# Performance work log

Measured on AMD Instinct MI355X. Metric: run time of the kernel, lower is better.

## Reference

```python
import jax, jax.numpy as jnp
import numpy as np

HIDDEN = 5120
NH = 32
DQ = 128    # qk nope dim
DR = 64     # qk rope dim
DV = 128    # v head dim
Q_LORA = 1536
KV_LORA = 512
T = 2048
THETA = 10000.0
EPS = 1e-6


def rmsnorm(x, g, eps=EPS):
    return x * jax.lax.rsqrt(jnp.mean(x * x, axis=-1, keepdims=True) + eps) * g


def rotate_gptj(x):
    # interleaved pairs: (x0, x1) -> (-x1, x0)
    x1 = x[..., ::2]
    x2 = x[..., 1::2]
    return jnp.stack((-x2, x1), axis=-1).reshape(x.shape)


def setup_inputs() -> dict:
    key = jax.random.key(0)
    ks = jax.random.split(key, 8)
    s = 0.02
    return {
        'positions': jnp.arange(T, dtype=jnp.int32),
        'hidden_states': jax.random.normal(ks[0], (T, HIDDEN), jnp.float32),
        'w_qa': jax.random.normal(ks[1], (HIDDEN, Q_LORA), jnp.float32) * s,
        'gamma_q': jnp.ones((Q_LORA,), jnp.float32),
        'w_qb': jax.random.normal(ks[2], (Q_LORA, NH * (DQ + DR)), jnp.float32) * s,
        'w_kva': jax.random.normal(ks[3], (HIDDEN, KV_LORA + DR), jnp.float32) * s,
        'gamma_kv': jnp.ones((KV_LORA,), jnp.float32),
        'w_kvb': jax.random.normal(ks[4], (KV_LORA, NH * (DQ + DV)), jnp.float32) * s,
        'w_o': jax.random.normal(ks[5], (NH * DV, HIDDEN), jnp.float32) * s,
    }


def reference(positions, hidden_states, w_qa, gamma_q, w_qb, w_kva, gamma_kv, w_kvb, w_o):
    t = hidden_states.shape[0]
    # --- Q path: low-rank down-proj, RMSNorm, up-proj ---
    q_c = rmsnorm(hidden_states @ w_qa, gamma_q)               # [T, Q_LORA]
    q = (q_c @ w_qb).reshape(t, NH, DQ + DR)                   # [T, H, 192]
    q_nope, q_pe = q[..., :DQ], q[..., DQ:]
    # --- KV path: joint down-proj, split latent / rope key, RMSNorm latent ---
    kv = hidden_states @ w_kva                                 # [T, KV_LORA + DR]
    kv_c, k_pe = kv[:, :KV_LORA], kv[:, KV_LORA:]
    kv_c = rmsnorm(kv_c, gamma_kv)
    kv_up = (kv_c @ w_kvb).reshape(t, NH, DQ + DV)             # [T, H, 256]
    k_nope, v = kv_up[..., :DQ], kv_up[..., DQ:]
    # --- partial RoPE (GPT-J rotate, neox-style cos/sin cache) ---
    inv_freq = 1.0 / (THETA ** (jnp.arange(0, DR, 2, dtype=jnp.float32) / DR))
    freqs = positions.astype(jnp.float32)[:, None] * inv_freq  # [T, DR/2]
    emb = jnp.concatenate((freqs, freqs), axis=-1)             # [T, DR]
    cos = jnp.cos(emb)[:, None, :]                             # [T, 1, DR]
    sin = jnp.sin(emb)[:, None, :]
    q_pe = q_pe * cos + rotate_gptj(q_pe) * sin                # [T, H, DR]
    k_pe = k_pe[:, None, :]
    k_pe = k_pe * cos + rotate_gptj(k_pe) * sin                # [T, 1, DR]
    # --- attention ---
    q_full = jnp.concatenate((q_nope, q_pe), axis=-1)                          # [T, H, 192]
    k_full = jnp.concatenate((k_nope, jnp.broadcast_to(k_pe, (t, NH, DR))), axis=-1)
    scale = (DQ + DR) ** -0.5
    scores = jnp.einsum('qhd,khd->hqk', q_full, k_full) * scale                # [H, T, T]
    causal = positions[:, None] >= positions[None, :]
    scores = jnp.where(causal[None], scores, jnp.float32(-1e30))
    attn = jax.nn.softmax(scores, axis=-1)
    out = jnp.einsum('hqk,khd->qhd', attn, v).reshape(t, NH * DV)              # [T, H*DV]
    return out @ w_o                                                           # [T, HIDDEN]
```

## Files before the change

### kernel.cpp

```cpp
#include <hip/hip_runtime.h>
#include <hip/hip_bf16.h>
#include <cstdint>
#include <cstddef>

#define T_SEQ   2048
#define HIDDEN  5120
#define NH      32
#define DQ      128
#define DR      64
#define DV      128
#define Q_LORA  1536
#define KV_LORA 512
#define QD      (DQ + DR)
#define KVD     (KV_LORA + DR)
#define QROW    (NH * QD)
#define KVUPROW (NH * (DQ + DV))
#define AOROW   (NH * DV)
#define FUSED_N (Q_LORA + KVD)
#define FUSED_PE (Q_LORA + KV_LORA)

typedef short bf16x8 __attribute__((ext_vector_type(8)));
typedef float f32x4  __attribute__((ext_vector_type(4)));

#define GLOAD16(gp, lp)                                                        \
    __builtin_amdgcn_global_load_lds(                                          \
        (const __attribute__((address_space(1))) void*)(gp),                   \
        (__attribute__((address_space(3))) void*)(lp), 16, 0, 0)

static __device__ __forceinline__ short f2bf(float f)
{
    union { float f; unsigned u; } v; v.f = f;
    unsigned r = v.u + 0x7FFFu + ((v.u >> 16) & 1u);
    return (short)(r >> 16);
}
static __device__ __forceinline__ float bf2f(short s)
{
    union { unsigned u; float f; } v;
    v.u = ((unsigned)(unsigned short)s) << 16;
    return v.f;
}

__global__ __launch_bounds__(256) void zero_f32(float* __restrict__ p, int n4)
{
    const int stride = gridDim.x * 256;
    for (int i = blockIdx.x * 256 + threadIdx.x; i < n4; i += stride)
        ((float4*)p)[i] = make_float4(0.f, 0.f, 0.f, 0.f);
}

__global__ __launch_bounds__(256) void conv_bf(
    const float* __restrict__ src, short* __restrict__ dst)
{
    const size_t i = ((size_t)blockIdx.x * 256 + threadIdx.x) * 8;
    float4 a = *(const float4*)&src[i];
    float4 b = *(const float4*)&src[i + 4];
    union { short s[8]; uint4 u; } o;
    o.s[0] = f2bf(a.x); o.s[1] = f2bf(a.y); o.s[2] = f2bf(a.z); o.s[3] = f2bf(a.w);
    o.s[4] = f2bf(b.x); o.s[5] = f2bf(b.y); o.s[6] = f2bf(b.z); o.s[7] = f2bf(b.w);
    *(uint4*)&dst[i] = o.u;
}

__global__ __launch_bounds__(256) void tr_f32_bf16(
    const float* __restrict__ src, short* __restrict__ dst, int K, int N)
{
    const int k0 = blockIdx.x * 32, n0 = blockIdx.y * 32;
    __shared__ float t[32][33];
    const int tid = threadIdx.x;
    {
        const int r = tid >> 3, c4 = (tid & 7) * 4;
        float4 v = *(const float4*)&src[(size_t)(k0 + r) * N + n0 + c4];
        t[r][c4 + 0] = v.x; t[r][c4 + 1] = v.y;
        t[r][c4 + 2] = v.z; t[r][c4 + 3] = v.w;
    }
    __syncthreads();
    {
        const int n = tid >> 3, k4 = (tid & 7) * 4;
        union { short s[4]; uint2 u; } o;
#pragma unroll
        for (int j = 0; j < 4; ++j) o.s[j] = f2bf(t[k4 + j][n]);
        *(uint2*)&dst[(size_t)(n0 + n) * K + k0 + k4] = o.u;
    }
}

__global__ __launch_bounds__(256, 4) void gemm_bt(
    const short* __restrict__ A, const short* __restrict__ BT,
    float* __restrict__ Cf, short* __restrict__ Cb, int N, int K,
    int lda, int ldbt, int ldc)
{
    __shared__ short As[128 * 64];
    __shared__ short Bs[128 * 64];

    const int gx = gridDim.x;
    const int nwg = gx * gridDim.y;
    int flat = blockIdx.y * gx + blockIdx.x;
    if ((nwg & 7) == 0) {
        const int chunk = nwg >> 3;
        flat = (flat & 7) * chunk + (flat >> 3);
    }
    const int bm = (flat / gx) * 128;
    const int bn = (flat % gx) * 128;

    const int kchunk = K / gridDim.z;
    const int kbeg   = kchunk * blockIdx.z;
    const int kend   = kbeg + kchunk;

    const int tid  = threadIdx.x;
    const int w    = tid >> 6;
    const int l    = tid & 63;
    const int wm   = (w >> 1) * 64;
    const int wn   = (w & 1) * 64;
    const int quad = l >> 4;
    const int lrow = l & 15;

    f32x4 acc[4][4];
#pragma unroll
    for (int mt = 0; mt < 4; ++mt)
#pragma unroll
        for (int nt = 0; nt < 4; ++nt)
            acc[mt][nt] = (f32x4){0.f, 0.f, 0.f, 0.f};

    const int r0  = tid >> 3;
    const int c8  = (tid & 7) * 8;
    const int rbA = bm + r0;
    int rbB = bn + r0; if (rbB > N - 1) rbB = N - 1;

    for (int k0 = kbeg; k0 < kend; k0 += 64) {
        __syncthreads();
#pragma unroll
        for (int i = 0; i < 4; ++i) {
            const int r = r0 + 32 * i;
            GLOAD16(&A[(size_t)(rbA + 32 * i) * lda + k0 + c8], &As[r * 64 + c8]);
        }
#pragma unroll
        for (int i = 0; i < 4; ++i) {
            const int r  = r0 + 32 * i;
            int rb = rbB + 32 * i; if (rb > N - 1) rb = N - 1;
            GLOAD16(&BT[(size_t)rb * ldbt + k0 + c8], &Bs[r * 64 + c8]);
        }
        __syncthreads();

#pragma unroll
        for (int ks = 0; ks < 2; ++ks) {
            bf16x8 af[4], bfr[4];
#pragma unroll
            for (int mt = 0; mt < 4; ++mt)
                af[mt] = *(const bf16x8*)&As[(wm + mt * 16 + lrow) * 64 + ks * 32 + quad * 8];
#pragma unroll
            for (int nt = 0; nt < 4; ++nt)
                bfr[nt] = *(const bf16x8*)&Bs[(wn + nt * 16 + lrow) * 64 + ks * 32 + quad * 8];
#pragma unroll
            for (int mt = 0; mt < 4; ++mt)
#pragma unroll
                for (int nt = 0; nt < 4; ++nt)
                    acc[mt][nt] = __builtin_amdgcn_mfma_f32_16x16x32_bf16(
                        af[mt], bfr[nt], acc[mt][nt], 0, 0, 0);
        }
    }

    if (Cb == nullptr) {
        const bool atom = (gridDim.z > 1);
#pragma unroll
        for (int mt = 0; mt < 4; ++mt)
#pragma unroll
            for (int i = 0; i < 4; ++i) {
                const int row = bm + wm + mt * 16 + quad * 4 + i;
                float* crow = Cf + (size_t)row * ldc;
#pragma unroll
                for (int nt = 0; nt < 4; ++nt) {
                    const int col = bn + wn + nt * 16 + lrow;
                    if (col < N) {
                        if (atom) atomicAdd(&crow[col], acc[mt][nt][i]);
                        else      crow[col] = acc[mt][nt][i];
                    }
                }
            }
    } else {
#pragma unroll
        for (int mt = 0; mt < 4; ++mt)
#pragma unroll
            for (int i = 0; i < 4; ++i) {
                const int row = bm + wm + mt * 16 + quad * 4 + i;
                short* crow = Cb + (size_t)row * ldc;
#pragma unroll
                for (int nt = 0; nt < 4; ++nt) {
                    const int col = bn + wn + nt * 16 + lrow;
                    if (col < N) crow[col] = f2bf(acc[mt][nt][i]);
                }
            }
    }
}

__global__ __launch_bounds__(256, 4) void gemm_kv(
    const short* __restrict__ A, const short* __restrict__ BT,
    short* __restrict__ Kg, short* __restrict__ Vg)
{
    __shared__ short As[128 * 64];
    __shared__ short Bs[128 * 64];

    const int gx = gridDim.x;
    const int nwg = gx * gridDim.y;
    int flat = blockIdx.y * gx + blockIdx.x;
    if ((nwg & 7) == 0) {
        const int chunk = nwg >> 3;
        flat = (flat & 7) * chunk + (flat >> 3);
    }
    const int bm = (flat / gx) * 128;
    const int bn = (flat % gx) * 128;

    const int tid  = threadIdx.x;
    const int w    = tid >> 6;
    const int l    = tid & 63;
    const int wm   = (w >> 1) * 64;
    const int wn   = (w & 1) * 64;
    const int quad = l >> 4;
    const int lrow = l & 15;

    f32x4 acc[4][4];
#pragma unroll
    for (int mt = 0; mt < 4; ++mt)
#pragma unroll
        for (int nt = 0; nt < 4; ++nt)
            acc[mt][nt] = (f32x4){0.f, 0.f, 0.f, 0.f};

    const int r0 = tid >> 3;
    const int c8 = (tid & 7) * 8;

    for (int k0 = 0; k0 < KV_LORA; k0 += 64) {
        __syncthreads();
#pragma unroll
        for (int i = 0; i < 4; ++i) {
            const int r = r0 + 32 * i;
            GLOAD16(&A[(size_t)(bm + r) * KV_LORA + k0 + c8], &As[r * 64 + c8]);
        }
#pragma unroll
        for (int i = 0; i < 4; ++i) {
            const int r = r0 + 32 * i;
            GLOAD16(&BT[(size_t)(bn + r) * KV_LORA + k0 + c8], &Bs[r * 64 + c8]);
        }
        __syncthreads();

#pragma unroll
        for (int ks = 0; ks < 2; ++ks) {
            bf16x8 af[4], bfr[4];
#pragma unroll
            for (int mt = 0; mt < 4; ++mt)
                af[mt] = *(const bf16x8*)&As[(wm + mt * 16 + lrow) * 64 + ks * 32 + quad * 8];
#pragma unroll
            for (int nt = 0; nt < 4; ++nt)
                bfr[nt] = *(const bf16x8*)&Bs[(wn + nt * 16 + lrow) * 64 + ks * 32 + quad * 8];
#pragma unroll
            for (int mt = 0; mt < 4; ++mt)
#pragma unroll
                for (int nt = 0; nt < 4; ++nt)
                    acc[mt][nt] = __builtin_amdgcn_mfma_f32_16x16x32_bf16(
                        af[mt], bfr[nt], acc[mt][nt], 0, 0, 0);
        }
    }

    const int  h     = bn >> 8;
    const bool vhalf = (bn & 128) != 0;
    if (!vhalf) {
        short* KgH = Kg + (size_t)h * (2048 * 192);
#pragma unroll
        for (int mt = 0; mt < 4; ++mt)
#pragma unroll
            for (int i = 0; i < 4; ++i) {
                const int row = bm + wm + mt * 16 + quad * 4 + i;
#pragma unroll
                for (int nt = 0; nt < 4; ++nt) {
                    const int d = wn + nt * 16 + lrow;
                    KgH[(size_t)row * 192 + d] = f2bf(acc[mt][nt][i]);
                }
            }
    } else {
        short* VgH = Vg + (size_t)h * (128 * 2048);
#pragma unroll
        for (int mt = 0; mt < 4; ++mt)
#pragma unroll
            for (int nt = 0; nt < 4; ++nt) {
                const int dv   = wn + nt * 16 + lrow;
                const int rowb = bm + wm + mt * 16 + quad * 4;
                union { short s[4]; uint2 u; } t;
                t.s[0] = f2bf(acc[mt][nt][0]); t.s[1] = f2bf(acc[mt][nt][1]);
                t.s[2] = f2bf(acc[mt][nt][2]); t.s[3] = f2bf(acc[mt][nt][3]);
                *(uint2*)&VgH[(size_t)dv * 2048 + rowb] = t.u;
            }
    }
}

__global__ __launch_bounds__(256) void rmsnorm_bf(
    const float* __restrict__ x, const float* __restrict__ g,
    short* __restrict__ y, int len, int in_stride, int out_stride)
{
    const float* xr = x + (size_t)blockIdx.x * in_stride;
    short*       yr = y + (size_t)blockIdx.x * out_stride;
    float ss = 0.f;
    for (int i = threadIdx.x; i < len; i += 256) {
        float v = xr[i];
        ss += v * v;
    }
#pragma unroll
    for (int off = 32; off > 0; off >>= 1) ss += __shfl_down(ss, off);
    __shared__ float red[4];
    if ((threadIdx.x & 63) == 0) red[threadIdx.x >> 6] = ss;
    __syncthreads();
    float tot = red[0] + red[1] + red[2] + red[3];
    float scale = rsqrtf(tot / (float)len + 1e-6f);
    for (int i = threadIdx.x; i < len; i += 256)
        yr[i] = f2bf(xr[i] * scale * g[i]);
}

#define ROPE_LN_THETA_OVER_32 0.28782313662425575f

__device__ __forceinline__ void rope_pair(float p, int i, float& x0, float& x1)
{
    const int   j0 = (2 * i) & 31;
    const int   j1 = (2 * i + 1) & 31;
    const float a0 = p * expf(-(float)j0 * ROPE_LN_THETA_OVER_32);
    const float a1 = p * expf(-(float)j1 * ROPE_LN_THETA_OVER_32);
    const float r0 = x0 * cosf(a0) - x1 * sinf(a0);
    const float r1 = x1 * cosf(a1) + x0 * sinf(a1);
    x0 = r0; x1 = r1;
}

__global__ __launch_bounds__(256) void rope_q_bf(
    short* __restrict__ qb, const int* __restrict__ pos)
{
    const int idx = blockIdx.x * 256 + threadIdx.x;
    const int i = idx & 31;
    const int h = (idx >> 5) & 31;
    const int t = idx >> 10;
    short* base = qb + (size_t)t * QROW + h * QD + DQ;
    float x0 = bf2f(base[2 * i]), x1 = bf2f(base[2 * i + 1]);
    rope_pair((float)pos[t], i, x0, x1);
    union { short s[2]; unsigned u; } o;
    o.s[0] = f2bf(x0); o.s[1] = f2bf(x1);
    *(unsigned*)&base[2 * i] = o.u;
}

__global__ __launch_bounds__(256) void rope_k_bcast(
    const float* __restrict__ qkva, const int* __restrict__ pos,
    short* __restrict__ Kg)
{
    const int idx = blockIdx.x * 256 + threadIdx.x;
    const int i = idx & 31;
    const int t = idx >> 5;
    const float* base = qkva + (size_t)t * FUSED_N + FUSED_PE;
    float x0 = base[2 * i], x1 = base[2 * i + 1];
    rope_pair((float)pos[t], i, x0, x1);
    union { short s[2]; unsigned u; } pk;
    pk.s[0] = f2bf(x0); pk.s[1] = f2bf(x1);
    for (int h = 0; h < NH; ++h)
        *(unsigned*)&Kg[((size_t)h * 2048 + t) * 192 + 128 + 2 * i] = pk.u;
}

__global__ __launch_bounds__(256) void attn_mfma(
    const short* __restrict__ qb, const short* __restrict__ Kg,
    const short* __restrict__ Vg, short* __restrict__ aout)
{
    const int h  = blockIdx.x;
    const int qb_ = blockIdx.y;
    const int q0 = qb_ * 64;

    __shared__ short Qs[64 * 200];
    __shared__ short Ks[64 * 200];
    __shared__ short Vt[128 * 72];
    __shared__ short Ps[64 * 72];

    const int tid  = threadIdx.x;
    const int w    = tid >> 6;
    const int l    = tid & 63;
    const int quad = l >> 4;
    const int lrow = l & 15;

    const float scale = 0.07216878364870322f;

#pragma unroll
    for (int it = 0; it < 6; ++it) {
        const int id = tid + 256 * it;
        const int r = id / 24, g = id % 24;
        *(uint4*)&Qs[r * 200 + g * 8] =
            *(const uint4*)&qb[(size_t)(q0 + r) * QROW + h * QD + g * 8];
    }
    __syncthreads();

    bf16x8 afq[6];
#pragma unroll
    for (int ks = 0; ks < 6; ++ks)
        afq[ks] = *(const bf16x8*)&Qs[(w * 16 + lrow) * 200 + ks * 32 + quad * 8];

    f32x4 Oacc[8];
#pragma unroll
    for (int nt = 0; nt < 8; ++nt) Oacc[nt] = (f32x4){0.f, 0.f, 0.f, 0.f};
    float m_run[4] = {-1e30f, -1e30f, -1e30f, -1e30f};
    float l_run[4] = {0.f, 0.f, 0.f, 0.f};

    const short* KgH = Kg + (size_t)h * (2048 * 192);
    const short* VgH = Vg + (size_t)h * (128 * 2048);

    for (int kt = 0; kt <= qb_; ++kt) {
        __syncthreads();
#pragma unroll
        for (int it = 0; it < 6; ++it) {
            const int id = tid + 256 * it;
            const int r = id / 24, g = id % 24;
            *(uint4*)&Ks[r * 200 + g * 8] =
                *(const uint4*)&KgH[(size_t)(kt * 64 + r) * 192 + g * 8];
        }
#pragma unroll
        for (int it = 0; it < 4; ++it) {
            const int id = tid + 256 * it;
            const int rv = id >> 3, g = id & 7;
            *(uint4*)&Vt[rv * 72 + g * 8] =
                *(const uint4*)&VgH[(size_t)rv * 2048 + kt * 64 + g * 8];
        }
        __syncthreads();

        f32x4 Sc[4];
#pragma unroll
        for (int nt = 0; nt < 4; ++nt) Sc[nt] = (f32x4){0.f, 0.f, 0.f, 0.f};
#pragma unroll
        for (int ks = 0; ks < 6; ++ks)
#pragma unroll
            for (int nt = 0; nt < 4; ++nt) {
                bf16x8 bk = *(const bf16x8*)&Ks[(nt * 16 + lrow) * 200 + ks * 32 + quad * 8];
                Sc[nt] = __builtin_amdgcn_mfma_f32_16x16x32_bf16(afq[ks], bk, Sc[nt], 0, 0, 0);
            }
#pragma unroll
        for (int nt = 0; nt < 4; ++nt)
#pragma unroll
            for (int i = 0; i < 4; ++i) Sc[nt][i] *= scale;

        if (kt == qb_) {
            const int qrow = w * 16 + quad * 4;
#pragma unroll
            for (int nt = 0; nt < 4; ++nt)
#pragma unroll
                for (int i = 0; i < 4; ++i)
                    if (nt * 16 + lrow > qrow + i) Sc[nt][i] = -1e30f;
        }

        float alpha[4];
#pragma unroll
        for (int i = 0; i < 4; ++i) {
            float m = fmaxf(fmaxf(Sc[0][i], Sc[1][i]), fmaxf(Sc[2][i], Sc[3][i]));
            m = fmaxf(m, __shfl_xor(m, 1));
            m = fmaxf(m, __shfl_xor(m, 2));
            m = fmaxf(m, __shfl_xor(m, 4));
            m = fmaxf(m, __shfl_xor(m, 8));
            const float mn = fmaxf(m_run[i], m);
            alpha[i] = expf(m_run[i] - mn);
            m_run[i] = mn;
        }

        float rs[4] = {0.f, 0.f, 0.f, 0.f};
#pragma unroll
        for (int nt = 0; nt < 4; ++nt)
#pragma unroll
            for (int i = 0; i < 4; ++i) {
                const float p = expf(Sc[nt][i] - m_run[i]);
                rs[i] += p;
                Ps[(w * 16 + quad * 4 + i) * 72 + nt * 16 + lrow] = f2bf(p);
            }
#pragma unroll
        for (int i = 0; i < 4; ++i) {
            float r = rs[i];
            r += __shfl_xor(r, 1);
            r += __shfl_xor(r, 2);
            r += __shfl_xor(r, 4);
            r += __shfl_xor(r, 8);
            l_run[i] = l_run[i] * alpha[i] + r;
        }

#pragma unroll
        for (int nt = 0; nt < 8; ++nt)
#pragma unroll
            for (int i = 0; i < 4; ++i) Oacc[nt][i] *= alpha[i];

#pragma unroll
        for (int ks2 = 0; ks2 < 2; ++ks2) {
            bf16x8 ap = *(const bf16x8*)&Ps[(w * 16 + lrow) * 72 + ks2 * 32 + quad * 8];
#pragma unroll
            for (int nt = 0; nt < 8; ++nt) {
                bf16x8 bv = *(const bf16x8*)&Vt[(nt * 16 + lrow) * 72 + ks2 * 32 + quad * 8];
                Oacc[nt] = __builtin_amdgcn_mfma_f32_16x16x32_bf16(ap, bv, Oacc[nt], 0, 0, 0);
            }
        }
    }

    float invl[4];
#pragma unroll
    for (int i = 0; i < 4; ++i) invl[i] = 1.f / l_run[i];
#pragma unroll
    for (int nt = 0; nt < 8; ++nt)
#pragma unroll
        for (int i = 0; i < 4; ++i)
            aout[(size_t)(q0 + w * 16 + quad * 4 + i) * AOROW + h * 128 + nt * 16 + lrow]
                = f2bf(Oacc[nt][i] * invl[i]);
}

extern "C" void kernel_launch(void* const* d_in, const int* in_sizes, int n_in,
                              void* d_out, int out_size, void* d_ws, size_t ws_size,
                              hipStream_t stream)
{
    const int*   positions = (const int*)d_in[0];
    const float* hidden    = (const float*)d_in[1];
    const float* w_qa      = (const float*)d_in[2];
    const float* gamma_q   = (const float*)d_in[3];
    const float* w_qb      = (const float*)d_in[4];
    const float* w_kva     = (const float*)d_in[5];
    const float* gamma_kv  = (const float*)d_in[6];
    const float* w_kvb     = (const float*)d_in[7];
    const float* w_o       = (const float*)d_in[8];
    float*       out       = (float*)d_out;

    short* wT      = (short*)d_ws;
    short* hid_bf  = wT      + (size_t)20971520;
    short* qbuf_bf = hid_bf  + (size_t)T_SEQ * HIDDEN;
    short* Kg      = qbuf_bf + (size_t)T_SEQ * QROW;
    short* Vg      = Kg      + (size_t)NH * 2048 * 192;
    short* aout_bf = Vg      + (size_t)NH * 128 * 2048;
    short* qa_bf   = aout_bf + (size_t)T_SEQ * AOROW;
    short* kvc_bf  = qa_bf   + (size_t)T_SEQ * Q_LORA;
    float* qkva    = (float*)Vg;

    const dim3 blk(256);

    zero_f32<<<dim3(2048), blk, 0, stream>>>(qkva, T_SEQ * FUSED_N / 4);
    zero_f32<<<dim3(2048), blk, 0, stream>>>(out, T_SEQ * HIDDEN / 4);
    conv_bf<<<dim3(T_SEQ * HIDDEN / 8 / 256), blk, 0, stream>>>(hidden, hid_bf);

    tr_f32_bf16<<<dim3(HIDDEN / 32, Q_LORA / 32), blk, 0, stream>>>(w_qa, wT, HIDDEN, Q_LORA);
    tr_f32_bf16<<<dim3(HIDDEN / 32, KVD / 32), blk, 0, stream>>>(
        w_kva, wT + (size_t)Q_LORA * HIDDEN, HIDDEN, KVD);
    gemm_bt<<<dim3((FUSED_N + 127) / 128, T_SEQ / 128, 2), blk, 0, stream>>>(
        hid_bf, wT, qkva, nullptr, FUSED_N, HIDDEN, HIDDEN, HIDDEN, FUSED_N);

    rmsnorm_bf<<<dim3(T_SEQ), blk, 0, stream>>>(qkva, gamma_q, qa_bf, Q_LORA, FUSED_N, Q_LORA);
    rmsnorm_bf<<<dim3(T_SEQ), blk, 0, stream>>>(qkva + Q_LORA, gamma_kv, kvc_bf,
                                                KV_LORA, FUSED_N, KV_LORA);
    rope_k_bcast<<<dim3(T_SEQ * 32 / 256), blk, 0, stream>>>(qkva, positions, Kg);

    tr_f32_bf16<<<dim3(Q_LORA / 32, QROW / 32), blk, 0, stream>>>(w_qb, wT, Q_LORA, QROW);
    gemm_bt<<<dim3(QROW / 128, T_SEQ / 128, 1), blk, 0, stream>>>(
        qa_bf, wT, nullptr, qbuf_bf, QROW, Q_LORA, Q_LORA, Q_LORA, QROW);

    tr_f32_bf16<<<dim3(KV_LORA / 32, KVUPROW / 32), blk, 0, stream>>>(w_kvb, wT, KV_LORA, KVUPROW);
    gemm_kv<<<dim3(KVUPROW / 128, T_SEQ / 128), blk, 0, stream>>>(kvc_bf, wT, Kg, Vg);

    rope_q_bf<<<dim3(T_SEQ * NH * 32 / 256), blk, 0, stream>>>(qbuf_bf, positions);

    attn_mfma<<<dim3(NH, T_SEQ / 64), blk, 0, stream>>>(qbuf_bf, Kg, Vg, aout_bf);

    tr_f32_bf16<<<dim3(AOROW / 32, HIDDEN / 32), blk, 0, stream>>>(w_o, wT, AOROW, HIDDEN);
    gemm_bt<<<dim3(HIDDEN / 128, T_SEQ / 128, 2), blk, 0, stream>>>(
        aout_bf, wT, out, nullptr, HIDDEN, AOROW, AOROW, AOROW, HIDDEN);
}
```

Measured before the change: 758.7 us.

## Prefetch next K/V tile into registers, fold scale into exp2, reverse block order

```diff
diff --git a/kernel.cpp b/kernel.cpp
--- a/kernel.cpp
+++ b/kernel.cpp
@@ -357,11 +357,10 @@
     const short* __restrict__ qb, const short* __restrict__ Kg,
     const short* __restrict__ Vg, short* __restrict__ aout)
 {
-    const int h  = blockIdx.x;
-    const int qb_ = blockIdx.y;
-    const int q0 = qb_ * 64;
-
-    __shared__ short Qs[64 * 200];
+    const int h   = blockIdx.x;
+    const int qb_ = gridDim.y - 1 - blockIdx.y;
+    const int q0  = qb_ * 64;
+
     __shared__ short Ks[64 * 200];
     __shared__ short Vt[128 * 72];
     __shared__ short Ps[64 * 72];
@@ -372,30 +371,38 @@
     const int quad = l >> 4;
     const int lrow = l & 15;
 
-    const float scale = 0.07216878364870322f;
-
+    const float K2 = 0.104117547f;
+
+    bf16x8 afq[6];
+    {
+        const short* qrow = qb + (size_t)(q0 + w * 16 + lrow) * QROW + h * QD;
+#pragma unroll
+        for (int ks = 0; ks < 6; ++ks)
+            afq[ks] = *(const bf16x8*)&qrow[ks * 32 + quad * 8];
+    }
+
+    f32x4 Oacc[8];
+#pragma unroll
+    for (int nt = 0; nt < 8; ++nt) Oacc[nt] = (f32x4){0.f, 0.f, 0.f, 0.f};
+    float m_run[4] = {-1e30f, -1e30f, -1e30f, -1e30f};
+    float l_run[4] = {0.f, 0.f, 0.f, 0.f};
+
+    const short* KgH = Kg + (size_t)h * (2048 * 192);
+    const short* VgH = Vg + (size_t)h * (128 * 2048);
+
+    uint4 kreg[6], vreg[4];
 #pragma unroll
     for (int it = 0; it < 6; ++it) {
         const int id = tid + 256 * it;
         const int r = id / 24, g = id % 24;
-        *(uint4*)&Qs[r * 200 + g * 8] =
-            *(const uint4*)&qb[(size_t)(q0 + r) * QROW + h * QD + g * 8];
-    }
-    __syncthreads();
-
-    bf16x8 afq[6];
-#pragma unroll
-    for (int ks = 0; ks < 6; ++ks)
-        afq[ks] = *(const bf16x8*)&Qs[(w * 16 + lrow) * 200 + ks * 32 + quad * 8];
-
-    f32x4 Oacc[8];
-#pragma unroll
-    for (int nt = 0; nt < 8; ++nt) Oacc[nt] = (f32x4){0.f, 0.f, 0.f, 0.f};
-    float m_run[4] = {-1e30f, -1e30f, -1e30f, -1e30f};
-    float l_run[4] = {0.f, 0.f, 0.f, 0.f};
-
-    const short* KgH = Kg + (size_t)h * (2048 * 192);
-    const short* VgH = Vg + (size_t)h * (128 * 2048);
+        kreg[it] = *(const uint4*)&KgH[(size_t)r * 192 + g * 8];
+    }
+#pragma unroll
+    for (int it = 0; it < 4; ++it) {
+        const int id = tid + 256 * it;
+        const int rv = id >> 3, g = id & 7;
+        vreg[it] = *(const uint4*)&VgH[(size_t)rv * 2048 + g * 8];
+    }
 
     for (int kt = 0; kt <= qb_; ++kt) {
         __syncthreads();
@@ -403,17 +410,30 @@
         for (int it = 0; it < 6; ++it) {
             const int id = tid + 256 * it;
             const int r = id / 24, g = id % 24;
-            *(uint4*)&Ks[r * 200 + g * 8] =
-                *(const uint4*)&KgH[(size_t)(kt * 64 + r) * 192 + g * 8];
+            *(uint4*)&Ks[r * 200 + g * 8] = kreg[it];
         }
 #pragma unroll
         for (int it = 0; it < 4; ++it) {
             const int id = tid + 256 * it;
             const int rv = id >> 3, g = id & 7;
-            *(uint4*)&Vt[rv * 72 + g * 8] =
-                *(const uint4*)&VgH[(size_t)rv * 2048 + kt * 64 + g * 8];
+            *(uint4*)&Vt[rv * 72 + g * 8] = vreg[it];
         }
         __syncthreads();
+
+        if (kt < qb_) {
+#pragma unroll
+            for (int it = 0; it < 6; ++it) {
+                const int id = tid + 256 * it;
+                const int r = id / 24, g = id % 24;
+                kreg[it] = *(const uint4*)&KgH[(size_t)((kt + 1) * 64 + r) * 192 + g * 8];
+            }
+#pragma unroll
+            for (int it = 0; it < 4; ++it) {
+                const int id = tid + 256 * it;
+                const int rv = id >> 3, g = id & 7;
+                vreg[it] = *(const uint4*)&VgH[(size_t)rv * 2048 + (kt + 1) * 64 + g * 8];
+            }
+        }
 
         f32x4 Sc[4];
 #pragma unroll
@@ -425,10 +445,6 @@
                 bf16x8 bk = *(const bf16x8*)&Ks[(nt * 16 + lrow) * 200 + ks * 32 + quad * 8];
                 Sc[nt] = __builtin_amdgcn_mfma_f32_16x16x32_bf16(afq[ks], bk, Sc[nt], 0, 0, 0);
             }
-#pragma unroll
-        for (int nt = 0; nt < 4; ++nt)
-#pragma unroll
-            for (int i = 0; i < 4; ++i) Sc[nt][i] *= scale;
 
         if (kt == qb_) {
             const int qrow = w * 16 + quad * 4;
@@ -439,7 +455,7 @@
                     if (nt * 16 + lrow > qrow + i) Sc[nt][i] = -1e30f;
         }
 
-        float alpha[4];
+        float alpha[4], negmk[4];
 #pragma unroll
         for (int i = 0; i < 4; ++i) {
             float m = fmaxf(fmaxf(Sc[0][i], Sc[1][i]), fmaxf(Sc[2][i], Sc[3][i]));
@@ -448,7 +464,8 @@
             m = fmaxf(m, __shfl_xor(m, 4));
             m = fmaxf(m, __shfl_xor(m, 8));
             const float mn = fmaxf(m_run[i], m);
-            alpha[i] = expf(m_run[i] - mn);
+            negmk[i] = -mn * K2;
+            alpha[i] = exp2f(fmaf(m_run[i], K2, negmk[i]));
             m_run[i] = mn;
         }
 
@@ -457,7 +474,7 @@
         for (int nt = 0; nt < 4; ++nt)
 #pragma unroll
             for (int i = 0; i < 4; ++i) {
-                const float p = expf(Sc[nt][i] - m_run[i]);
+                const float p = exp2f(fmaf(Sc[nt][i], K2, negmk[i]));
                 rs[i] += p;
                 Ps[(w * 16 + quad * 4 + i) * 72 + nt * 16 + lrow] = f2bf(p);
             }
```

After: 841.0 us. +10.8%, slower.
